# Performance work log

Hardware: AMD Instinct MI355X
Metric: run time of the kernel (lower is better)

Reference implementation:

```python
import jax, jax.numpy as jnp
import numpy as np

D_MODEL = 512
TEMP = 30.0  # softmax temperature used by TransformerTrack-style RelationUnit
EPS = 1e-5
NORM_SCALE = float(np.sqrt(1.0 / (D_MODEL * 4 * 4)))


def _instance_l2norm(x):
    # x: [n, hw, b, d]; InstanceL2Norm over (dim, h, w) per (image, batch) sample
    n, hw, b, d = x.shape
    ss = jnp.sum(x * x, axis=(1, 3), keepdims=True)  # [n,1,b,1]
    return x * (NORM_SCALE * jnp.sqrt((d * hw) / (ss + EPS)))


def _cnorm(r, i):
    # joint L2 normalization of a complex vector along last axis
    s = jnp.sqrt(jnp.sum(r * r + i * i, axis=-1, keepdims=True) + 1e-12)
    return r / s, i / s


def _rel_self_attn(xr, xi, er, ei, WK):
    # xr/xi: [n, L, b, d]; er/ei: [n, L, L, b, dk] relative (helix) embeddings
    qr, qi = _cnorm(xr @ WK, xi @ WK)           # [n,L,b,dk]
    # real part of complex conjugate inner product <q, k>
    scores = (jnp.einsum('nqbk,nlbk->nbql', qr, qr)
              + jnp.einsum('nqbk,nlbk->nbql', qi, qi)
              + jnp.einsum('nqbk,nqlbk->nbql', qr, er)
              + jnp.einsum('nqbk,nqlbk->nbql', qi, ei))
    A = jax.nn.softmax(scores * TEMP, axis=-1)  # [n,b,q,l]
    out_r = jnp.einsum('nbql,nlbd->nqbd', A, xr)
    out_i = jnp.einsum('nbql,nlbd->nqbd', A, xi)
    return out_r, out_i


def _cross_attn(qr_in, qi_in, kr_in, ki_in, vr, vi, WK):
    # q: [Lq,b,d]; k,v: [Lk,b,d]
    qr, qi = _cnorm(qr_in @ WK, qi_in @ WK)
    kr, ki = _cnorm(kr_in @ WK, ki_in @ WK)
    scores = jnp.einsum('qbk,lbk->bql', qr, kr) + jnp.einsum('qbk,lbk->bql', qi, ki)
    A = jax.nn.softmax(scores * TEMP, axis=-1)
    out_r = jnp.einsum('bql,lbd->qbd', A, vr)
    out_i = jnp.einsum('bql,lbd->qbd', A, vi)
    return out_r, out_i


def _forward(src_real, src_imag, tgt_real, tgt_imag,
             src_emb_real, src_emb_imag, tgt_emb_real, tgt_emb_imag,
             pos_real, pos_imag, WK_rel, WK_cross):
    n, b, d, h, w = src_real.shape
    hw = h * w

    def tok(x):  # [n,b,d,h,w] -> [n,hw,b,d]
        return x.reshape(n, b, d, hw).transpose(0, 3, 1, 2)

    def emb(x):  # [n,b,dk,hw,hw] -> [n,hw,hw,b,dk]
        return x.transpose(0, 3, 4, 1, 2)

    sr, si = tok(src_real), tok(src_imag)
    tr, ti = tok(tgt_real), tok(tgt_imag)
    esr, esi = emb(src_emb_real), emb(src_emb_imag)
    etr, eti = emb(tgt_emb_real), emb(tgt_emb_imag)

    # ---- encoder (num_layers = 1) ----
    s2r, s2i = _rel_self_attn(sr, si, esr, esi, WK_rel)
    mem_r = _instance_l2norm(sr + s2r).reshape(n * hw, b, d)
    mem_i = _instance_l2norm(si + s2i).reshape(n * hw, b, d)

    # pos: [n,b,h,w] -> [n*hw, b, d] (broadcast over dim as in .repeat(1,1,dim))
    pr = jnp.broadcast_to(pos_real.reshape(n, b, hw).transpose(0, 2, 1).reshape(n * hw, b, 1), (n * hw, b, d))
    pi = jnp.broadcast_to(pos_imag.reshape(n, b, hw).transpose(0, 2, 1).reshape(n * hw, b, 1), (n * hw, b, d))

    def IN3(x):
        return _instance_l2norm(x.reshape(n, hw, b, d)).reshape(n * hw, b, d)

    # ---- decoder (num_layers = 1) ----
    t2r, t2i = _rel_self_attn(tr, ti, etr, eti, WK_rel)
    xr = _instance_l2norm(tr + t2r).reshape(n * hw, b, d)
    xi = _instance_l2norm(ti + t2i).reshape(n * hw, b, d)

    mask_r, mask_i = _cross_attn(xr, xi, mem_r, mem_i, pr, pi, WK_cross)
    y2r = IN3(xr * mask_r)
    y2i = IN3(xi * mask_i)

    t3r, t3i = _cross_attn(xr, xi, mem_r, mem_i, mem_r * pr, mem_i * pi, WK_cross)
    y4r = IN3(xr + t3r)
    y4i = IN3(xi + t3i)

    out_r = IN3(y2r + y4r)
    out_i = IN3(y2i + y4i)

    feat_r = out_r.reshape(n, h, w, b, d).transpose(0, 3, 4, 1, 2).reshape(n * b, d, h, w)
    feat_i = out_i.reshape(n, h, w, b, d).transpose(0, 3, 4, 1, 2).reshape(n * b, d, h, w)
    return out_r, out_i, feat_r, feat_i


def setup_inputs() -> dict:
    key = jax.random.key(0)
    ks = jax.random.split(key, 12)
    n, b, d, h, dk = 2, 2, 512, 16, 64
    hw = h * h
    inp = {
        'src_real': jax.random.normal(ks[0], (n, b, d, h, h), jnp.float32),
        'src_imag': jax.random.normal(ks[1], (n, b, d, h, h), jnp.float32),
        'tgt_real': jax.random.normal(ks[2], (n, b, d, h, h), jnp.float32),
        'tgt_imag': jax.random.normal(ks[3], (n, b, d, h, h), jnp.float32),
        'src_emb_real': jax.random.normal(ks[4], (n, b, dk, hw, hw), jnp.float32),
        'src_emb_imag': jax.random.normal(ks[5], (n, b, dk, hw, hw), jnp.float32),
        'tgt_emb_real': jax.random.normal(ks[6], (n, b, dk, hw, hw), jnp.float32),
        'tgt_emb_imag': jax.random.normal(ks[7], (n, b, dk, hw, hw), jnp.float32),
        'pos_real': jax.random.uniform(ks[8], (n, b, h, h), jnp.float32),
        'pos_imag': jax.random.uniform(ks[9], (n, b, h, h), jnp.float32),
        'WK_rel': jax.random.normal(ks[10], (d, dk), jnp.float32) * 0.02,
        'WK_cross': jax.random.normal(ks[11], (d, 128), jnp.float32) * 0.02,
    }
    return inp


def reference(src_real, src_imag, tgt_real, tgt_imag,
              src_emb_real, src_emb_imag, tgt_emb_real, tgt_emb_imag,
              pos_real, pos_imag, WK_rel, WK_cross):
    return _forward(src_real, src_imag, tgt_real, tgt_imag,
                    src_emb_real, src_emb_imag, tgt_emb_real, tgt_emb_imag,
                    pos_real, pos_imag, WK_rel, WK_cross)
```

## Files before the change

kernel.cpp:

```cpp
#include <hip/hip_runtime.h>
#include <cstdint>
#include <cstddef>

#define N_ 2
#define B_ 2
#define D_ 512
#define HW_ 256
#define DK_ 64
#define DKC_ 128
#define G_ 4
#define NBLK_ 32

constexpr size_t OFF_TSR = 0;
constexpr size_t OFF_TSI = 524288;
constexpr size_t OFF_TTR = 1048576;
constexpr size_t OFF_TTI = 1572864;
constexpr size_t OFF_QSR = 2097152;
constexpr size_t OFF_QSI = OFF_QSR + 65536;
constexpr size_t OFF_QTR = OFF_QSI + 65536;
constexpr size_t OFF_QTI = OFF_QTR + 65536;
constexpr size_t OFF_AS  = OFF_QTI + 65536;
constexpr size_t OFF_AT  = OFF_AS + 262144;
constexpr size_t OFF_YSR = OFF_AT + 262144;
constexpr size_t OFF_YSI = OFF_YSR + 524288;
constexpr size_t OFF_YTR = OFF_YSI + 524288;
constexpr size_t OFF_YTI = OFF_YTR + 524288;
constexpr size_t OFF_QCR = OFF_YTI + 524288;
constexpr size_t OFF_QCI = OFF_QCR + 131072;
constexpr size_t OFF_KCR = OFF_QCI + 131072;
constexpr size_t OFF_KCI = OFF_KCR + 131072;
constexpr size_t OFF_AC  = OFF_KCI + 131072;
constexpr size_t OFF_T3R = OFF_AC + 524288;
constexpr size_t OFF_T3I = OFF_T3R + 524288;
constexpr size_t OFF_MR  = OFF_T3I + 524288;
constexpr size_t OFF_MI  = OFF_MR + 1024;
constexpr size_t OFF_P1  = OFF_MI + 1024;
constexpr size_t OFF_P2  = OFF_P1 + 512;
constexpr size_t OFF_P3  = OFF_P2 + 512;

template<int NT>
__device__ __forceinline__ float blk_sum(float v, float* sh) {
  int tid = threadIdx.x;
  sh[tid] = v; __syncthreads();
  #pragma unroll
  for (int s = NT/2; s > 0; s >>= 1) { if (tid < s) sh[tid] += sh[tid+s]; __syncthreads(); }
  float r = sh[0]; __syncthreads(); return r;
}
template<int NT>
__device__ __forceinline__ float blk_max(float v, float* sh) {
  int tid = threadIdx.x;
  sh[tid] = v; __syncthreads();
  #pragma unroll
  for (int s = NT/2; s > 0; s >>= 1) { if (tid < s) sh[tid] = fmaxf(sh[tid], sh[tid+s]); __syncthreads(); }
  float r = sh[0]; __syncthreads(); return r;
}
__device__ __forceinline__ float wave_sum32(float v) {
  #pragma unroll
  for (int o = 16; o; o >>= 1) v += __shfl_xor(v, o, 64);
  return v;
}
__device__ __forceinline__ float scale_from(const float* part, int q) {
  float ss = 0.f;
  #pragma unroll
  for (int j = 0; j < NBLK_; ++j) ss += part[q*NBLK_ + j];
  return 4.f * rsqrtf(ss + 1e-5f);
}

__global__ void k_transpose(const float* sR, const float* sI, const float* tR, const float* tI, float* ws) {
  int which = blockIdx.y;
  const float* in = (which==0)? sR : (which==1)? sI : (which==2)? tR : tI;
  float* out = ws + ((which==0)? OFF_TSR : (which==1)? OFF_TSI : (which==2)? OFF_TTR : OFF_TTI);
  int bx = blockIdx.x;
  int pt = bx & 3, dt = (bx>>2)&7, nb = bx>>5;
  int ni = nb>>1, bi = nb&1;
  __shared__ float tile[64][65];
  int tid = threadIdx.x;
  int p0 = pt*64, d0 = dt*64;
  #pragma unroll
  for (int it=0; it<16; ++it) {
    int i = it*256 + tid; int row = i>>6, col = i&63;
    tile[row][col] = in[(size_t)(nb*D_ + d0+row)*HW_ + p0+col];
  }
  __syncthreads();
  #pragma unroll
  for (int it=0; it<16; ++it) {
    int i = it*256 + tid; int row = i>>6, col = i&63;
    out[(size_t)((ni*HW_ + p0+row)*B_ + bi)*D_ + d0+col] = tile[col][row];
  }
}

__global__ void __launch_bounds__(256) k_qrel(float* ws, const float* WK) {
  int bx = blockIdx.x;
  int rg = bx & 127, which = bx >> 7;
  const float* Tr = ws + (which ? OFF_TTR : OFF_TSR);
  const float* Ti = ws + (which ? OFF_TTI : OFF_TSI);
  float* Qr = ws + (which ? OFF_QTR : OFF_QSR);
  float* Qi = ws + (which ? OFF_QTI : OFF_QSI);
  int R0 = rg*8;
  __shared__ float Xr[8][512], Xi[8][512];
  int tid = threadIdx.x;
  const float4* tr4 = (const float4*)(Tr + (size_t)R0*D_);
  const float4* ti4 = (const float4*)(Ti + (size_t)R0*D_);
  #pragma unroll
  for (int it=0; it<4; ++it) {
    int i = it*256 + tid;
    ((float4*)&Xr[0][0])[i] = tr4[i];
    ((float4*)&Xi[0][0])[i] = ti4[i];
  }
  __syncthreads();
  int row = tid >> 5, col2 = (tid & 31)*2;
  float a0r=0.f, a0i=0.f, a1r=0.f, a1i=0.f;
  #pragma unroll 4
  for (int d=0; d<512; ++d) {
    float2 w = *(const float2*)&WK[(size_t)d*DK_ + col2];
    float xr = Xr[row][d], xi = Xi[row][d];
    a0r += xr*w.x; a1r += xr*w.y;
    a0i += xi*w.x; a1i += xi*w.y;
  }
  float ss = wave_sum32(a0r*a0r + a1r*a1r + a0i*a0i + a1i*a1i);
  float inv = 1.f / sqrtf(ss + 1e-12f);
  size_t o = (size_t)(R0+row)*DK_ + col2;
  Qr[o]   = a0r*inv; Qr[o+1] = a1r*inv;
  Qi[o]   = a0i*inv; Qi[o+1] = a1i*inv;
}

__global__ void __launch_bounds__(128) k_gram(float* ws) {
  int bx = blockIdx.x;
  int lt = bx & 3, qt = (bx>>2)&7, nb = (bx>>5)&3, which = bx>>7;
  int ni = nb>>1, bi = nb&1;
  const float* Qr = ws + (which ? OFF_QTR : OFF_QSR);
  const float* Qi = ws + (which ? OFF_QTI : OFF_QSI);
  float* A = ws + (which ? OFF_AT : OFF_AS) + (size_t)nb*65536;
  __shared__ float Qrs[32][33], Qis[32][33], Krs[32][68], Kis[32][68];
  int tid = threadIdx.x, ty = tid>>4, tx = tid&15;
  int ty4 = ty*4, tx4 = tx*4;
  float acc[4][4] = {};
  for (int c = 0; c < 2; ++c) {
    #pragma unroll
    for (int it = 0; it < 8; ++it) {
      int i = it*128 + tid; int row = i>>5, col = i&31;
      size_t qa = (size_t)((ni*HW_ + qt*32+row)*B_ + bi)*DK_ + c*32 + col;
      Qrs[row][col] = Qr[qa];
      Qis[row][col] = Qi[qa];
    }
    #pragma unroll
    for (int it = 0; it < 16; ++it) {
      int i = it*128 + tid; int kk = i&31, col = i>>5;
      size_t ka = (size_t)((ni*HW_ + lt*64+col)*B_ + bi)*DK_ + c*32 + kk;
      Krs[kk][col] = Qr[ka];
      Kis[kk][col] = Qi[ka];
    }
    __syncthreads();
    #pragma unroll
    for (int kk = 0; kk < 32; ++kk) {
      float4 kr = *(const float4*)&Krs[kk][tx4];
      float4 ki = *(const float4*)&Kis[kk][tx4];
      #pragma unroll
      for (int i = 0; i < 4; ++i) {
        float qr = Qrs[ty4+i][kk], qi = Qis[ty4+i][kk];
        acc[i][0] += qr*kr.x + qi*ki.x;
        acc[i][1] += qr*kr.y + qi*ki.y;
        acc[i][2] += qr*kr.z + qi*ki.z;
        acc[i][3] += qr*kr.w + qi*ki.w;
      }
    }
    __syncthreads();
  }
  #pragma unroll
  for (int i = 0; i < 4; ++i)
    #pragma unroll
    for (int j = 0; j < 4; ++j)
      A[(size_t)(qt*32+ty4+i)*256 + lt*64+tx4+j] = acc[i][j];
}

#define LOAD4(BR, BI, C)                                         \
  _Pragma("unroll")                                              \
  for (int t = 0; t < 4; ++t) {                                  \
    BR[t] = er4[(size_t)((C)*4 + t) * 16384];                    \
    BI[t] = ei4[(size_t)((C)*4 + t) * 16384];                    \
  }                                                              \
  __builtin_amdgcn_sched_barrier(0);
#define CONS4(BR, BI, K0)                                        \
  _Pragma("unroll")                                              \
  for (int t = 0; t < 4; ++t) {                                  \
    float fr = __shfl(qvr, (K0) + t);                            \
    float fi = __shfl(qvi, (K0) + t);                            \
    a0 += fr*BR[t].x + fi*BI[t].x;                               \
    a1 += fr*BR[t].y + fi*BI[t].y;                               \
    a2 += fr*BR[t].z + fi*BI[t].z;                               \
    a3 += fr*BR[t].w + fi*BI[t].w;                               \
  }                                                              \
  __builtin_amdgcn_sched_barrier(0);

__global__ void __launch_bounds__(256, 4) k_selfattn(float* ws, const float* esr, const float* esi,
                                                     const float* etr, const float* eti) {
  int idx = blockIdx.x;
  int iq = idx & 255, nb = (idx>>8)&3, which = idx>>10;
  int ni = nb>>1, bi = nb&1;
  const float* Qr = ws + (which ? OFF_QTR : OFF_QSR);
  const float* Qi = ws + (which ? OFF_QTI : OFF_QSI);
  const float* er = which ? etr : esr;
  const float* ei = which ? eti : esi;
  float* Arow = ws + (which ? OFF_AT : OFF_AS) + (size_t)nb*65536 + (size_t)iq*256;
  int tid = threadIdx.x, w = tid>>6, lane = tid&63;
  int tokq = ni*HW_ + iq;
  int kl = lane & 15;
  float qvr = Qr[(size_t)(tokq*B_ + bi)*DK_ + w*16 + kl];
  float qvi = Qi[(size_t)(tokq*B_ + bi)*DK_ + w*16 + kl];
  int l0 = lane*4;
  size_t eb = (size_t)nb*4194304 + (size_t)(w*16)*65536 + (size_t)iq*256 + l0;
  const float4* er4 = (const float4*)&er[eb];
  const float4* ei4 = (const float4*)&ei[eb];
  float4 Ra[4], Ia[4], Rb[4], Ib[4];
  float a0=0.f, a1=0.f, a2=0.f, a3=0.f;
  LOAD4(Ra, Ia, 0)
  LOAD4(Rb, Ib, 1)
  CONS4(Ra, Ia, 0)
  LOAD4(Ra, Ia, 2)
  CONS4(Rb, Ib, 4)
  LOAD4(Rb, Ib, 3)
  CONS4(Ra, Ia, 8)
  CONS4(Rb, Ib, 12)
  __shared__ float part[4][256];
  __shared__ float sh[256];
  *(float4*)&part[w][l0] = make_float4(a0,a1,a2,a3);
  __syncthreads();
  float s = (part[0][tid]+part[1][tid]+part[2][tid]+part[3][tid] + Arow[tid]) * 30.f;
  float m = blk_max<256>(s, sh);
  float e = __expf(s - m);
  float sum = blk_sum<256>(e, sh);
  Arow[tid] = e / sum;
}

__global__ void __launch_bounds__(128) k_selfapply(float* ws) {
  int bx = blockIdx.x;
  int dt = bx & 7, qt = (bx>>3)&7, nb = (bx>>6)&3, which = bx>>8;
  int ni = nb>>1, bi = nb&1;
  const float* A  = ws + (which ? OFF_AT : OFF_AS) + (size_t)nb*65536;
  const float* Xr = ws + (which ? OFF_TTR : OFF_TSR);
  const float* Xi = ws + (which ? OFF_TTI : OFF_TSI);
  float* Yr = ws + (which ? OFF_YTR : OFF_YSR);
  float* Yi = ws + (which ? OFF_YTI : OFF_YSI);
  __shared__ float As[32][33], Xrs[32][68], Xis[32][68];
  int tid = threadIdx.x, ty = tid>>4, tx = tid&15;
  int ty4 = ty*4, tx4 = tx*4;
  float ar[4][4] = {}, ai[4][4] = {};
  for (int c = 0; c < 8; ++c) {
    #pragma unroll
    for (int it = 0; it < 8; ++it) {
      int i = it*128 + tid; int row = i>>5, col = i&31;
      As[row][col] = A[(size_t)(qt*32+row)*256 + c*32+col];
    }
    #pragma unroll
    for (int it = 0; it < 16; ++it) {
      int i = it*128 + tid; int row = i>>6, col = i&63;
      size_t xb = (size_t)((ni*HW_ + c*32+row)*B_ + bi)*D_ + dt*64+col;
      Xrs[row][col] = Xr[xb]; Xis[row][col] = Xi[xb];
    }
    __syncthreads();
    #pragma unroll
    for (int kk = 0; kk < 32; ++kk) {
      float4 vr = *(const float4*)&Xrs[kk][tx4];
      float4 vi = *(const float4*)&Xis[kk][tx4];
      #pragma unroll
      for (int i = 0; i < 4; ++i) {
        float a = As[ty4+i][kk];
        ar[i][0] += a*vr.x; ar[i][1] += a*vr.y; ar[i][2] += a*vr.z; ar[i][3] += a*vr.w;
        ai[i][0] += a*vi.x; ai[i][1] += a*vi.y; ai[i][2] += a*vi.z; ai[i][3] += a*vi.w;
      }
    }
    __syncthreads();
  }
  #pragma unroll
  for (int i = 0; i < 4; ++i) {
    size_t o = (size_t)((ni*HW_ + qt*32 + ty4+i)*B_ + bi)*D_ + dt*64 + tx4;
    #pragma unroll
    for (int j = 0; j < 4; ++j) { Yr[o+j] = Xr[o+j] + ar[i][j]; Yi[o+j] = Xi[o+j] + ai[i][j]; }
  }
}

__global__ void k_reduce4(float* ws) {
  int qy = blockIdx.y;
  const float* a = ws + ((qy==0)? OFF_YSR : (qy==1)? OFF_YSI : (qy==2)? OFF_YTR : OFF_YTI);
  int g = blockIdx.x / NBLK_, blk = blockIdx.x % NBLK_;
  int ni = g>>1, bi = g&1;
  int tid = threadIdx.x;
  float acc = 0.f;
  for (int p = blk; p < HW_; p += NBLK_) {
    const float* row = a + (size_t)((ni*HW_ + p)*B_ + bi)*D_;
    for (int d = tid; d < D_; d += 256) { float v = row[d]; acc += v*v; }
  }
  __shared__ float sh[256];
  float s = blk_sum<256>(acc, sh);
  if (!tid) ws[OFF_P1 + (size_t)(qy*G_ + g)*NBLK_ + blk] = s;
}

__global__ void __launch_bounds__(256) k_crossproj(float* ws, const float* W) {
  int bx = blockIdx.x;
  int rg = bx & 127, isK = bx >> 7;
  const float* inR = ws + (isK ? OFF_YSR : OFF_YTR);
  const float* inI = ws + (isK ? OFF_YSI : OFF_YTI);
  float* oR = ws + (isK ? OFF_KCR : OFF_QCR);
  float* oI = ws + (isK ? OFF_KCI : OFF_QCI);
  int R0 = rg*8;
  __shared__ float Xr[8][512], Xi[8][512];
  int tid = threadIdx.x;
  const float4* xr4 = (const float4*)(inR + (size_t)R0*D_);
  const float4* xi4 = (const float4*)(inI + (size_t)R0*D_);
  #pragma unroll
  for (int it=0; it<4; ++it) {
    int i = it*256 + tid;
    ((float4*)&Xr[0][0])[i] = xr4[i];
    ((float4*)&Xi[0][0])[i] = xi4[i];
  }
  __syncthreads();
  int row = tid >> 5, col4 = (tid & 31)*4;
  float ar[4]={}, ai[4]={};
  #pragma unroll 4
  for (int d=0; d<512; ++d) {
    float4 w = *(const float4*)&W[(size_t)d*DKC_ + col4];
    float xr = Xr[row][d], xi = Xi[row][d];
    ar[0] += xr*w.x; ar[1] += xr*w.y; ar[2] += xr*w.z; ar[3] += xr*w.w;
    ai[0] += xi*w.x; ai[1] += xi*w.y; ai[2] += xi*w.z; ai[3] += xi*w.w;
  }
  int rr = R0 + row;
  int bi = rr & 1, gg = ((rr>>1)>>8)*2 + bi;
  float sR = scale_from(ws + OFF_P1, (isK?0:2)*G_ + gg);
  float sI = scale_from(ws + OFF_P1, (isK?1:3)*G_ + gg);
  ar[0]*=sR; ar[1]*=sR; ar[2]*=sR; ar[3]*=sR;
  ai[0]*=sI; ai[1]*=sI; ai[2]*=sI; ai[3]*=sI;
  float ps = ar[0]*ar[0]+ar[1]*ar[1]+ar[2]*ar[2]+ar[3]*ar[3]
           + ai[0]*ai[0]+ai[1]*ai[1]+ai[2]*ai[2]+ai[3]*ai[3];
  float ss = wave_sum32(ps);
  float inv = 1.f / sqrtf(ss + 1e-12f);
  size_t o = (size_t)rr*DKC_ + col4;
  oR[o]   = ar[0]*inv; oR[o+1] = ar[1]*inv; oR[o+2] = ar[2]*inv; oR[o+3] = ar[3]*inv;
  oI[o]   = ai[0]*inv; oI[o+1] = ai[1]*inv; oI[o+2] = ai[2]*inv; oI[o+3] = ai[3]*inv;
}

__global__ void __launch_bounds__(128) k_crossscore(float* ws) {
  int bx = blockIdx.x;
  int lt = bx & 7, qt = (bx>>3)&15, bi = bx>>7;
  const float* Qr = ws + OFF_QCR; const float* Qi = ws + OFF_QCI;
  const float* Kr = ws + OFF_KCR; const float* Ki = ws + OFF_KCI;
  float* S = ws + OFF_AC + (size_t)bi*262144;
  __shared__ float Qrs[32][33], Qis[32][33], Krs[32][68], Kis[32][68];
  int tid = threadIdx.x, ty = tid>>4, tx = tid&15;
  int ty4 = ty*4, tx4 = tx*4;
  float acc[4][4] = {};
  for (int c = 0; c < 4; ++c) {
    #pragma unroll
    for (int it = 0; it < 8; ++it) {
      int i = it*128 + tid; int row = i>>5, col = i&31;
      Qrs[row][col] = Qr[(size_t)((qt*32+row)*B_ + bi)*DKC_ + c*32 + col];
      Qis[row][col] = Qi[(size_t)((qt*32+row)*B_ + bi)*DKC_ + c*32 + col];
    }
    #pragma unroll
    for (int it = 0; it < 16; ++it) {
      int i = it*128 + tid; int kk = i&31, col = i>>5;
      Krs[kk][col] = Kr[(size_t)((lt*64+col)*B_ + bi)*DKC_ + c*32 + kk];
      Kis[kk][col] = Ki[(size_t)((lt*64+col)*B_ + bi)*DKC_ + c*32 + kk];
    }
    __syncthreads();
    #pragma unroll
    for (int kk = 0; kk < 32; ++kk) {
      float4 kr = *(const float4*)&Krs[kk][tx4];
      float4 ki = *(const float4*)&Kis[kk][tx4];
      #pragma unroll
      for (int i = 0; i < 4; ++i) {
        float qr = Qrs[ty4+i][kk], qi = Qis[ty4+i][kk];
        acc[i][0] += qr*kr.x + qi*ki.x;
        acc[i][1] += qr*kr.y + qi*ki.y;
        acc[i][2] += qr*kr.z + qi*ki.z;
        acc[i][3] += qr*kr.w + qi*ki.w;
      }
    }
    __syncthreads();
  }
  #pragma unroll
  for (int i = 0; i < 4; ++i)
    #pragma unroll
    for (int j = 0; j < 4; ++j)
      S[(size_t)(qt*32+ty4+i)*512 + lt*64+tx4+j] = acc[i][j];
}

__global__ void k_softmaxrow(float* ws, const float* posr, const float* posi) {
  int bx = blockIdx.x;
  int bi = bx >> 9, iq = bx & 511;
  float* row = ws + OFF_AC + (size_t)bi*262144 + (size_t)iq*512;
  int tid = threadIdx.x;
  float s0 = row[tid]*30.f, s1 = row[tid+256]*30.f;
  __shared__ float sh[256];
  float m = blk_max<256>(fmaxf(s0, s1), sh);
  float e0 = __expf(s0 - m), e1 = __expf(s1 - m);
  float sum = blk_sum<256>(e0 + e1, sh);
  float inv = 1.f / sum;
  float a0 = e0*inv, a1 = e1*inv;
  row[tid] = a0; row[tid+256] = a1;
  float pr0 = posr[bi*HW_ + tid],        pr1 = posr[(B_+bi)*HW_ + tid];
  float pi0 = posi[bi*HW_ + tid],        pi1 = posi[(B_+bi)*HW_ + tid];
  float mr = blk_sum<256>(a0*pr0 + a1*pr1, sh);
  float mi = blk_sum<256>(a0*pi0 + a1*pi1, sh);
  if (!tid) { ws[OFF_MR + bi*512 + iq] = mr; ws[OFF_MI + bi*512 + iq] = mi; }
}

__global__ void __launch_bounds__(128) k_crossapply(float* ws, const float* posr, const float* posi) {
  int bx = blockIdx.x;
  int dt = bx & 7, qt = (bx>>3)&15, bi = (bx>>7)&1, kc = bx>>8;
  const float* A  = ws + OFF_AC + (size_t)bi*262144;
  const float* Mr = ws + OFF_YSR; const float* Mi = ws + OFF_YSI;
  float* Pr = ws + (kc ? OFF_TSR : OFF_T3R);
  float* Pi = ws + (kc ? OFF_TSI : OFF_T3I);
  float smr = scale_from(ws + OFF_P1, 0*G_ + kc*2 + bi);
  float smi = scale_from(ws + OFF_P1, 1*G_ + kc*2 + bi);
  __shared__ float As[32][33], Vrs[32][68], Vis[32][68];
  int tid = threadIdx.x, ty = tid>>4, tx = tid&15;
  int ty4 = ty*4, tx4 = tx*4;
  float ar[4][4] = {}, ai[4][4] = {};
  for (int c = 0; c < 8; ++c) {
    int kb = kc*256 + c*32;
    #pragma unroll
    for (int it = 0; it < 8; ++it) {
      int i = it*128 + tid; int row = i>>5, col = i&31;
      As[row][col] = A[(size_t)(qt*32+row)*512 + kb+col];
    }
    #pragma unroll
    for (int it = 0; it < 16; ++it) {
      int i = it*128 + tid; int row = i>>6, col = i&63;
      int l = kb + row; int pl = l & 255;
      float pvr = posr[(kc*B_ + bi)*HW_ + pl] * smr;
      float pvi = posi[(kc*B_ + bi)*HW_ + pl] * smi;
      size_t vb = (size_t)(l*B_ + bi)*D_ + dt*64+col;
      Vrs[row][col] = Mr[vb] * pvr;
      Vis[row][col] = Mi[vb] * pvi;
    }
    __syncthreads();
    #pragma unroll
    for (int kk = 0; kk < 32; ++kk) {
      float4 vr = *(const float4*)&Vrs[kk][tx4];
      float4 vi = *(const float4*)&Vis[kk][tx4];
      #pragma unroll
      for (int i = 0; i < 4; ++i) {
        float a = As[ty4+i][kk];
        ar[i][0] += a*vr.x; ar[i][1] += a*vr.y; ar[i][2] += a*vr.z; ar[i][3] += a*vr.w;
        ai[i][0] += a*vi.x; ai[i][1] += a*vi.y; ai[i][2] += a*vi.z; ai[i][3] += a*vi.w;
      }
    }
    __syncthreads();
  }
  #pragma unroll
  for (int i = 0; i < 4; ++i) {
    size_t o = (size_t)((qt*32+ty4+i)*B_ + bi)*D_ + dt*64 + tx4;
    #pragma unroll
    for (int j = 0; j < 4; ++j) { Pr[o+j] = ar[i][j]; Pi[o+j] = ai[i][j]; }
  }
}

__global__ void k_reducey24(float* ws) {
  int qy = blockIdx.y;
  int g = blockIdx.x / NBLK_, blk = blockIdx.x % NBLK_;
  int ni = g>>1, bi = g&1;
  const float* X   = ws + ((qy==0 || qy==2) ? OFF_YTR : OFF_YTI);
  const float* T3a = ws + ((qy==2) ? OFF_T3R : OFF_T3I);
  const float* T3b = ws + ((qy==2) ? OFF_TSR : OFF_TSI);
  const float* M   = ws + ((qy==0) ? OFF_MR : OFF_MI);
  float sx = scale_from(ws + OFF_P1, ((qy==0||qy==2) ? 2 : 3)*G_ + g);
  int tid = threadIdx.x;
  float acc = 0.f;
  for (int p = blk; p < HW_; p += NBLK_) {
    int l = ni*HW_ + p;
    size_t rb = (size_t)(l*B_ + bi)*D_;
    if (qy < 2) {
      float m = M[bi*512 + l] * sx;
      for (int d = tid; d < D_; d += 256) { float v = X[rb+d]*m; acc += v*v; }
    } else {
      for (int d = tid; d < D_; d += 256) { float v = X[rb+d]*sx + T3a[rb+d] + T3b[rb+d]; acc += v*v; }
    }
  }
  __shared__ float sh[256];
  float s = blk_sum<256>(acc, sh);
  if (!tid) ws[OFF_P2 + (size_t)(qy*G_ + g)*NBLK_ + blk] = s;
}

__global__ void k_combine(float* ws) {
  int y = blockIdx.y;
  int g = blockIdx.x / NBLK_, blk = blockIdx.x % NBLK_;
  int ni = g>>1, bi = g&1;
  const float* X   = ws + (y ? OFF_YTI : OFF_YTR);
  float* T3a       = ws + (y ? OFF_T3I : OFF_T3R);
  const float* T3b = ws + (y ? OFF_TSI : OFF_TSR);
  const float* M   = ws + (y ? OFF_MI : OFF_MR);
  float sx = scale_from(ws + OFF_P1, (2+y)*G_ + g);
  float a2 = scale_from(ws + OFF_P2, y*G_ + g);
  float a4 = scale_from(ws + OFF_P2, (2+y)*G_ + g);
  int tid = threadIdx.x;
  float acc = 0.f;
  for (int p = blk; p < HW_; p += NBLK_) {
    int l = ni*HW_ + p;
    float m = M[bi*512 + l];
    size_t rb = (size_t)(l*B_ + bi)*D_;
    for (int d = tid; d < D_; d += 256) {
      float x = X[rb+d] * sx;
      float z = a2*(x*m) + a4*(x + T3a[rb+d] + T3b[rb+d]);
      T3a[rb+d] = z;
      acc += z*z;
    }
  }
  __shared__ float sh[256];
  float s = blk_sum<256>(acc, sh);
  if (!tid) ws[OFF_P3 + (size_t)(y*G_ + g)*NBLK_ + blk] = s;
}

__global__ void k_final(float* ws, float* out) {
  int y = blockIdx.y;
  int bx = blockIdx.x;
  int pt = bx & 3, dt = (bx>>2)&7, nb = bx>>5;
  int ni = nb>>1, bi = nb&1;
  const float* Z = ws + (y ? OFF_T3I : OFF_T3R);
  float s = scale_from(ws + OFF_P3, y*G_ + nb);
  float* o1 = out + (size_t)y*524288;
  float* o2 = out + (size_t)(2+y)*524288;
  __shared__ float tile[64][65];
  int tid = threadIdx.x;
  int p0 = pt*64, d0 = dt*64;
  #pragma unroll
  for (int it = 0; it < 16; ++it) {
    int i = it*256 + tid; int row = i>>6, col = i&63;
    size_t idx = (size_t)((ni*HW_ + p0+row)*B_ + bi)*D_ + d0+col;
    float v = Z[idx] * s;
    o1[idx] = v;
    tile[row][col] = v;
  }
  __syncthreads();
  #pragma unroll
  for (int it = 0; it < 16; ++it) {
    int i = it*256 + tid; int row = i>>6, col = i&63;
    o2[(size_t)(nb*D_ + d0+row)*HW_ + p0+col] = tile[col][row];
  }
}

extern "C" void kernel_launch(void* const* d_in, const int* in_sizes, int n_in,
                              void* d_out, int out_size, void* d_ws, size_t ws_size,
                              hipStream_t stream) {
  const float* srcR = (const float*)d_in[0];
  const float* srcI = (const float*)d_in[1];
  const float* tgtR = (const float*)d_in[2];
  const float* tgtI = (const float*)d_in[3];
  const float* esr  = (const float*)d_in[4];
  const float* esi  = (const float*)d_in[5];
  const float* etr  = (const float*)d_in[6];
  const float* eti  = (const float*)d_in[7];
  const float* posR = (const float*)d_in[8];
  const float* posI = (const float*)d_in[9];
  const float* WKrel   = (const float*)d_in[10];
  const float* WKcross = (const float*)d_in[11];
  float* ws  = (float*)d_ws;
  float* out = (float*)d_out;

  k_transpose <<<dim3(128,4), 256, 0, stream>>>(srcR, srcI, tgtR, tgtI, ws);
  k_qrel      <<<256, 256, 0, stream>>>(ws, WKrel);
  k_gram      <<<256, 128, 0, stream>>>(ws);
  k_selfattn  <<<2048, 256, 0, stream>>>(ws, esr, esi, etr, eti);
  k_selfapply <<<512, 128, 0, stream>>>(ws);
  k_reduce4   <<<dim3(G_*NBLK_,4), 256, 0, stream>>>(ws);
  k_crossproj <<<256, 256, 0, stream>>>(ws, WKcross);
  k_crossscore<<<256, 128, 0, stream>>>(ws);
  k_softmaxrow<<<1024, 256, 0, stream>>>(ws, posR, posI);
  k_crossapply<<<512, 128, 0, stream>>>(ws, posR, posI);
  k_reducey24 <<<dim3(G_*NBLK_,4), 256, 0, stream>>>(ws);
  k_combine   <<<dim3(G_*NBLK_,2), 256, 0, stream>>>(ws);
  k_final     <<<dim3(128,2), 256, 0, stream>>>(ws, out);
}
```

Baseline: 283.9 us.

## Stream self-attention embeddings via async LDS ring and fuse norm reduction into apply

```diff
diff --git a/kernel.cpp b/kernel.cpp
--- a/kernel.cpp
+++ b/kernel.cpp
@@ -10,6 +10,8 @@
 #define DKC_ 128
 #define G_ 4
 #define NBLK_ 32
+
+typedef float f4 __attribute__((ext_vector_type(4)));
 
 constexpr size_t OFF_TSR = 0;
 constexpr size_t OFF_TSI = 524288;
@@ -35,7 +37,7 @@
 constexpr size_t OFF_MR  = OFF_T3I + 524288;
 constexpr size_t OFF_MI  = OFF_MR + 1024;
 constexpr size_t OFF_P1  = OFF_MI + 1024;
-constexpr size_t OFF_P2  = OFF_P1 + 512;
+constexpr size_t OFF_P2  = OFF_P1 + 1024;
 constexpr size_t OFF_P3  = OFF_P2 + 512;
 
 template<int NT>
@@ -59,11 +61,31 @@
   for (int o = 16; o; o >>= 1) v += __shfl_xor(v, o, 64);
   return v;
 }
+__device__ __forceinline__ float wave_sum64(float v) {
+  #pragma unroll
+  for (int o = 32; o; o >>= 1) v += __shfl_xor(v, o, 64);
+  return v;
+}
+__device__ __forceinline__ float wave_max64(float v) {
+  #pragma unroll
+  for (int o = 32; o; o >>= 1) v = fmaxf(v, __shfl_xor(v, o, 64));
+  return v;
+}
 __device__ __forceinline__ float scale_from(const float* part, int q) {
   float ss = 0.f;
   #pragma unroll
   for (int j = 0; j < NBLK_; ++j) ss += part[q*NBLK_ + j];
   return 4.f * rsqrtf(ss + 1e-5f);
+}
+__device__ __forceinline__ float scale_from64(const float* part, int q) {
+  float ss = 0.f;
+  #pragma unroll
+  for (int j = 0; j < 64; ++j) ss += part[q*64 + j];
+  return 4.f * rsqrtf(ss + 1e-5f);
+}
+__device__ __forceinline__ void gload16(const float* g, float* l) {
+  __builtin_amdgcn_global_load_lds((const __attribute__((address_space(1))) void*)g,
+                                   (__attribute__((address_space(3))) void*)l, 16, 0, 0);
 }
 
 __global__ void k_transpose(const float* sR, const float* sI, const float* tR, const float* tI, float* ws) {
@@ -173,63 +195,76 @@
       A[(size_t)(qt*32+ty4+i)*256 + lt*64+tx4+j] = acc[i][j];
 }
 
-#define LOAD4(BR, BI, C)                                         \
-  _Pragma("unroll")                                              \
-  for (int t = 0; t < 4; ++t) {                                  \
-    BR[t] = er4[(size_t)((C)*4 + t) * 16384];                    \
-    BI[t] = ei4[(size_t)((C)*4 + t) * 16384];                    \
-  }                                                              \
-  __builtin_amdgcn_sched_barrier(0);
-#define CONS4(BR, BI, K0)                                        \
-  _Pragma("unroll")                                              \
-  for (int t = 0; t < 4; ++t) {                                  \
-    float fr = __shfl(qvr, (K0) + t);                            \
-    float fi = __shfl(qvi, (K0) + t);                            \
-    a0 += fr*BR[t].x + fi*BI[t].x;                               \
-    a1 += fr*BR[t].y + fi*BI[t].y;                               \
-    a2 += fr*BR[t].z + fi*BI[t].z;                               \
-    a3 += fr*BR[t].w + fi*BI[t].w;                               \
-  }                                                              \
-  __builtin_amdgcn_sched_barrier(0);
-
-__global__ void __launch_bounds__(256, 4) k_selfattn(float* ws, const float* esr, const float* esi,
+__global__ void __launch_bounds__(256, 2) k_selfattn(float* ws, const float* esr, const float* esi,
                                                      const float* etr, const float* eti) {
+  __shared__ float ring[4][8][2][256];
   int idx = blockIdx.x;
-  int iq = idx & 255, nb = (idx>>8)&3, which = idx>>10;
+  int iqt = idx & 63, nb = (idx>>6)&3, which = idx>>8;
   int ni = nb>>1, bi = nb&1;
   const float* Qr = ws + (which ? OFF_QTR : OFF_QSR);
   const float* Qi = ws + (which ? OFF_QTI : OFF_QSI);
   const float* er = which ? etr : esr;
   const float* ei = which ? eti : esi;
+  int tid = threadIdx.x, w = tid>>6, lane = tid&63;
+  int iq = iqt*4 + w;
   float* Arow = ws + (which ? OFF_AT : OFF_AS) + (size_t)nb*65536 + (size_t)iq*256;
-  int tid = threadIdx.x, w = tid>>6, lane = tid&63;
   int tokq = ni*HW_ + iq;
-  int kl = lane & 15;
-  float qvr = Qr[(size_t)(tokq*B_ + bi)*DK_ + w*16 + kl];
-  float qvi = Qi[(size_t)(tokq*B_ + bi)*DK_ + w*16 + kl];
+  float qvr = Qr[(size_t)(tokq*B_ + bi)*DK_ + lane];
+  float qvi = Qi[(size_t)(tokq*B_ + bi)*DK_ + lane];
+  const float* gr = er + (size_t)nb*4194304 + (size_t)iq*256 + lane*4;
+  const float* gi = ei + (size_t)nb*4194304 + (size_t)iq*256 + lane*4;
+  unsigned ldsb = (unsigned)(size_t)(__attribute__((address_space(3))) char*)&ring[w][0][0][0]
+                + (unsigned)lane*16u;
+  #pragma unroll
+  for (int s = 0; s < 8; ++s) {
+    gload16(gr + (size_t)s*65536, &ring[w][s][0][0]);
+    gload16(gi + (size_t)s*65536, &ring[w][s][1][0]);
+  }
+  float a0=0.f, a1=0.f, a2=0.f, a3=0.f;
+#define STEP(u, GSTR, KK, DOISS)                                              \
+  { asm volatile("s_waitcnt vmcnt(" GSTR ")" ::: "memory");                   \
+    __builtin_amdgcn_sched_barrier(0);                                        \
+    f4 Rv, Iv;                                                                \
+    asm volatile("ds_read_b128 %0, %2\n\tds_read_b128 %1, %2 offset:1024"     \
+                 : "=v"(Rv), "=v"(Iv) : "v"(ldsb + (u)*2048u) : "memory");    \
+    asm volatile("s_waitcnt lgkmcnt(0)" ::: "memory");                        \
+    __builtin_amdgcn_sched_barrier(0);                                        \
+    if (DOISS) {                                                              \
+      gload16(gr + (size_t)((KK)+8)*65536, &ring[w][u][0][0]);                \
+      gload16(gi + (size_t)((KK)+8)*65536, &ring[w][u][1][0]);                \
+    }                                                                         \
+    float fr = __shfl(qvr, (KK)), fi = __shfl(qvi, (KK));                     \
+    a0 += fr*Rv[0] + fi*Iv[0];                                                \
+    a1 += fr*Rv[1] + fi*Iv[1];                                                \
+    a2 += fr*Rv[2] + fi*Iv[2];                                                \
+    a3 += fr*Rv[3] + fi*Iv[3];                                                \
+  }
+  for (int kb = 0; kb < 56; kb += 8) {
+    STEP(0, "14", kb+0, true)
+    STEP(1, "14", kb+1, true)
+    STEP(2, "14", kb+2, true)
+    STEP(3, "14", kb+3, true)
+    STEP(4, "14", kb+4, true)
+    STEP(5, "14", kb+5, true)
+    STEP(6, "14", kb+6, true)
+    STEP(7, "14", kb+7, true)
+  }
+  STEP(0, "14", 56, false)
+  STEP(1, "12", 57, false)
+  STEP(2, "10", 58, false)
+  STEP(3, "8",  59, false)
+  STEP(4, "6",  60, false)
+  STEP(5, "4",  61, false)
+  STEP(6, "2",  62, false)
+  STEP(7, "0",  63, false)
+#undef STEP
   int l0 = lane*4;
-  size_t eb = (size_t)nb*4194304 + (size_t)(w*16)*65536 + (size_t)iq*256 + l0;
-  const float4* er4 = (const float4*)&er[eb];
-  const float4* ei4 = (const float4*)&ei[eb];
-  float4 Ra[4], Ia[4], Rb[4], Ib[4];
-  float a0=0.f, a1=0.f, a2=0.f, a3=0.f;
-  LOAD4(Ra, Ia, 0)
-  LOAD4(Rb, Ib, 1)
-  CONS4(Ra, Ia, 0)
-  LOAD4(Ra, Ia, 2)
-  CONS4(Rb, Ib, 4)
-  LOAD4(Rb, Ib, 3)
-  CONS4(Ra, Ia, 8)
-  CONS4(Rb, Ib, 12)
-  __shared__ float part[4][256];
-  __shared__ float sh[256];
-  *(float4*)&part[w][l0] = make_float4(a0,a1,a2,a3);
-  __syncthreads();
-  float s = (part[0][tid]+part[1][tid]+part[2][tid]+part[3][tid] + Arow[tid]) * 30.f;
-  float m = blk_max<256>(s, sh);
-  float e = __expf(s - m);
-  float sum = blk_sum<256>(e, sh);
-  Arow[tid] = e / sum;
+  float4 g = *(const float4*)&Arow[l0];
+  float s0=(a0+g.x)*30.f, s1=(a1+g.y)*30.f, s2=(a2+g.z)*30.f, s3=(a3+g.w)*30.f;
+  float m = wave_max64(fmaxf(fmaxf(s0,s1), fmaxf(s2,s3)));
+  float e0=__expf(s0-m), e1=__expf(s1-m), e2=__expf(s2-m), e3=__expf(s3-m);
+  float inv = 1.f / wave_sum64(e0+e1+e2+e3);
+  *(float4*)&Arow[l0] = make_float4(e0*inv, e1*inv, e2*inv, e3*inv);
 }
 
 __global__ void __launch_bounds__(128) k_selfapply(float* ws) {
@@ -242,6 +277,7 @@
   float* Yr = ws + (which ? OFF_YTR : OFF_YSR);
   float* Yi = ws + (which ? OFF_YTI : OFF_YSI);
   __shared__ float As[32][33], Xrs[32][68], Xis[32][68];
+  __shared__ float red[128];
   int tid = threadIdx.x, ty = tid>>4, tx = tid&15;
   int ty4 = ty*4, tx4 = tx*4;
   float ar[4][4] = {}, ai[4][4] = {};
@@ -271,28 +307,24 @@
     }
     __syncthreads();
   }
+  float ssr = 0.f, ssi = 0.f;
   #pragma unroll
   for (int i = 0; i < 4; ++i) {
     size_t o = (size_t)((ni*HW_ + qt*32 + ty4+i)*B_ + bi)*D_ + dt*64 + tx4;
     #pragma unroll
-    for (int j = 0; j < 4; ++j) { Yr[o+j] = Xr[o+j] + ar[i][j]; Yi[o+j] = Xi[o+j] + ai[i][j]; }
-  }
-}
-
-__global__ void k_reduce4(float* ws) {
-  int qy = blockIdx.y;
-  const float* a = ws + ((qy==0)? OFF_YSR : (qy==1)? OFF_YSI : (qy==2)? OFF_YTR : OFF_YTI);
-  int g = blockIdx.x / NBLK_, blk = blockIdx.x % NBLK_;
-  int ni = g>>1, bi = g&1;
-  int tid = threadIdx.x;
-  float acc = 0.f;
-  for (int p = blk; p < HW_; p += NBLK_) {
-    const float* row = a + (size_t)((ni*HW_ + p)*B_ + bi)*D_;
-    for (int d = tid; d < D_; d += 256) { float v = row[d]; acc += v*v; }
-  }
-  __shared__ float sh[256];
-  float s = blk_sum<256>(acc, sh);
-  if (!tid) ws[OFF_P1 + (size_t)(qy*G_ + g)*NBLK_ + blk] = s;
+    for (int j = 0; j < 4; ++j) {
+      float yr = Xr[o+j] + ar[i][j];
+      float yi = Xi[o+j] + ai[i][j];
+      Yr[o+j] = yr; Yi[o+j] = yi;
+      ssr += yr*yr; ssi += yi*yi;
+    }
+  }
+  float tr_ = blk_sum<128>(ssr, red);
+  float ti_ = blk_sum<128>(ssi, red);
+  if (tid == 0) {
+    ws[OFF_P1 + (size_t)((which*2+0)*G_ + nb)*64 + qt*8 + dt] = tr_;
+    ws[OFF_P1 + (size_t)((which*2+1)*G_ + nb)*64 + qt*8 + dt] = ti_;
+  }
 }
 
 __global__ void __launch_bounds__(256) k_crossproj(float* ws, const float* W) {
@@ -325,8 +357,8 @@
   }
   int rr = R0 + row;
   int bi = rr & 1, gg = ((rr>>1)>>8)*2 + bi;
-  float sR = scale_from(ws + OFF_P1, (isK?0:2)*G_ + gg);
-  float sI = scale_from(ws + OFF_P1, (isK?1:3)*G_ + gg);
+  float sR = scale_from64(ws + OFF_P1, (isK?0:2)*G_ + gg);
+  float sI = scale_from64(ws + OFF_P1, (isK?1:3)*G_ + gg);
   ar[0]*=sR; ar[1]*=sR; ar[2]*=sR; ar[3]*=sR;
   ai[0]*=sI; ai[1]*=sI; ai[2]*=sI; ai[3]*=sI;
   float ps = ar[0]*ar[0]+ar[1]*ar[1]+ar[2]*ar[2]+ar[3]*ar[3]
@@ -411,8 +443,8 @@
   const float* Mr = ws + OFF_YSR; const float* Mi = ws + OFF_YSI;
   float* Pr = ws + (kc ? OFF_TSR : OFF_T3R);
   float* Pi = ws + (kc ? OFF_TSI : OFF_T3I);
-  float smr = scale_from(ws + OFF_P1, 0*G_ + kc*2 + bi);
-  float smi = scale_from(ws + OFF_P1, 1*G_ + kc*2 + bi);
+  float smr = scale_from64(ws + OFF_P1, 0*G_ + kc*2 + bi);
+  float smi = scale_from64(ws + OFF_P1, 1*G_ + kc*2 + bi);
   __shared__ float As[32][33], Vrs[32][68], Vis[32][68];
   int tid = threadIdx.x, ty = tid>>4, tx = tid&15;
   int ty4 = ty*4, tx4 = tx*4;
@@ -464,7 +496,7 @@
   const float* T3a = ws + ((qy==2) ? OFF_T3R : OFF_T3I);
   const float* T3b = ws + ((qy==2) ? OFF_TSR : OFF_TSI);
   const float* M   = ws + ((qy==0) ? OFF_MR : OFF_MI);
-  float sx = scale_from(ws + OFF_P1, ((qy==0||qy==2) ? 2 : 3)*G_ + g);
+  float sx = scale_from64(ws + OFF_P1, ((qy==0||qy==2) ? 2 : 3)*G_ + g);
   int tid = threadIdx.x;
   float acc = 0.f;
   for (int p = blk; p < HW_; p += NBLK_) {
@@ -490,7 +522,7 @@
   float* T3a       = ws + (y ? OFF_T3I : OFF_T3R);
   const float* T3b = ws + (y ? OFF_TSI : OFF_TSR);
   const float* M   = ws + (y ? OFF_MI : OFF_MR);
-  float sx = scale_from(ws + OFF_P1, (2+y)*G_ + g);
+  float sx = scale_from64(ws + OFF_P1, (2+y)*G_ + g);
   float a2 = scale_from(ws + OFF_P2, y*G_ + g);
   float a4 = scale_from(ws + OFF_P2, (2+y)*G_ + g);
   int tid = threadIdx.x;
@@ -560,9 +592,8 @@
   k_transpose <<<dim3(128,4), 256, 0, stream>>>(srcR, srcI, tgtR, tgtI, ws);
   k_qrel      <<<256, 256, 0, stream>>>(ws, WKrel);
   k_gram      <<<256, 128, 0, stream>>>(ws);
-  k_selfattn  <<<2048, 256, 0, stream>>>(ws, esr, esi, etr, eti);
+  k_selfattn  <<<512, 256, 0, stream>>>(ws, esr, esi, etr, eti);
   k_selfapply <<<512, 128, 0, stream>>>(ws);
-  k_reduce4   <<<dim3(G_*NBLK_,4), 256, 0, stream>>>(ws);
   k_crossproj <<<256, 256, 0, stream>>>(ws, WKcross);
   k_crossscore<<<256, 128, 0, stream>>>(ws);
   k_softmaxrow<<<1024, 256, 0, stream>>>(ws, posR, posI);
```

Result: slower. 292.6 us (+3.1%).
